# Performance work log

Hardware: AMD Instinct MI355X
Metric: run time of the kernel (lower is better)

Reference implementation:

```python
import jax, jax.numpy as jnp
import numpy as np

LN_EPS = 1e-5


def _pos_embed_2d(w, h, c, dtype=jnp.float32):
    # matches build_2d_sincos_position_embedding: meshgrid indexing='xy' -> (h, w) grids
    grid_w = jnp.arange(w, dtype=jnp.float32)
    grid_h = jnp.arange(h, dtype=jnp.float32)
    gw, gh = jnp.meshgrid(grid_w, grid_h, indexing='xy')  # each (h, w)
    pos_dim = c // 4
    omega = 1.0 / (10000.0 ** (jnp.arange(pos_dim, dtype=jnp.float32) / pos_dim))
    out_w = gw.reshape(-1, 1) * omega[None]  # (h*w, pos_dim)
    out_h = gh.reshape(-1, 1) * omega[None]
    pe = jnp.concatenate([jnp.sin(out_w), jnp.cos(out_w), jnp.sin(out_h), jnp.cos(out_h)], axis=1)
    return pe.astype(dtype)  # (h*w, c)


def setup_inputs() -> dict:
    key = jax.random.key(0)
    k1, k2 = jax.random.split(key)
    N, C, H, W = 16, 256, 40, 40
    x = jax.random.normal(k1, (N, C, H, W), dtype=jnp.float32)
    ln_w = jnp.ones((C,), dtype=jnp.float32)
    ln_b = jnp.zeros((C,), dtype=jnp.float32)
    qkv_w = jax.random.normal(k2, (3 * C, C), dtype=jnp.float32) * 0.02  # 1x1 conv weight
    qkv_b = jnp.zeros((3 * C,), dtype=jnp.float32)
    gamma = jnp.ones((1,), dtype=jnp.float32)
    return {"x": x, "ln_w": ln_w, "ln_b": ln_b, "qkv_w": qkv_w, "qkv_b": qkv_b, "gamma": gamma}


def reference(x, ln_w, ln_b, qkv_w, qkv_b, gamma):
    N, C, H, W = x.shape
    scale = C ** (-0.5)
    identity = x

    # LayerNorm over channels (computed in NHWC like the torch permute dance)
    xh = jnp.transpose(x, (0, 2, 3, 1))  # (N, H, W, C)
    mu = jnp.mean(xh, axis=-1, keepdims=True)
    var = jnp.mean(jnp.square(xh - mu), axis=-1, keepdims=True)
    xn = (xh - mu) * jax.lax.rsqrt(var + LN_EPS) * ln_w + ln_b

    # 1x1 conv == per-pixel linear
    qkv = jnp.einsum('nhwc,oc->nhwo', xn, qkv_w) + qkv_b  # (N, H, W, 3C)
    qkv = qkv.reshape(N, H * W, 3 * C)
    q, k, v = jnp.split(qkv, 3, axis=-1)  # each (N, HW, C)

    pe = _pos_embed_2d(W, H, C, x.dtype)  # (HW, C)
    q = q + pe
    k = k + pe

    attn = jax.nn.softmax(jnp.einsum('nqc,nkc->nqk', q, k) * scale, axis=-1)
    out = jnp.einsum('nqk,nkc->nqc', attn, v)  # (N, HW, C)
    out = jnp.transpose(out, (0, 2, 1)).reshape(N, C, H, W)
    return identity + gamma[0] * out
```

## Files before the change

kernel.cpp:

```cpp
#include <hip/hip_runtime.h>
#include <hip/hip_bf16.h>

typedef float f32x4 __attribute__((ext_vector_type(4)));
typedef float f32x16 __attribute__((ext_vector_type(16)));
typedef __bf16 v8bf __attribute__((ext_vector_type(8)));
typedef unsigned short ushortx4 __attribute__((ext_vector_type(4)));
typedef unsigned short ushortx8 __attribute__((ext_vector_type(8)));
typedef unsigned int uint4v __attribute__((ext_vector_type(4)));

#define NIMG 16
#define CCH  256
#define HWP  1600

#define QSCALE 0.09016844f
#define DEFER_THR 2.885390f

__device__ __forceinline__ unsigned short f2bf(float f) {
  unsigned int u = __builtin_bit_cast(unsigned int, f);
  u = (u + 0x7FFFu + ((u >> 16) & 1u)) >> 16;
  return (unsigned short)u;
}

__device__ __forceinline__ f32x4 mfma16(v8bf a, v8bf b, f32x4 c) {
  return __builtin_amdgcn_mfma_f32_16x16x32_bf16(a, b, c, 0, 0, 0);
}

__device__ __forceinline__ unsigned cvtpk(float a, float b) {
  unsigned r;
  asm("v_cvt_pk_bf16_f32 %0, %1, %2" : "=v"(r) : "v"(a), "v"(b));
  return r;
}
__device__ __forceinline__ float exp2v(float x) {
  float r;
  asm("v_exp_f32 %0, %1" : "=v"(r) : "v"(x));
  return r;
}
__device__ __forceinline__ float sin2pi(float rev) {
  float r;
  asm("v_fract_f32 %0, %1\n\tv_sin_f32 %0, %0" : "=v"(r) : "v"(rev));
  return r;
}
#define PSWAP(a, b) asm("v_permlane32_swap_b32 %0, %1" : "+v"(a), "+v"(b))

__global__ void prep_kernel(const float* __restrict__ qkv_w,
                            float* __restrict__ pe,
                            unsigned short* __restrict__ w_frag) {
  int tid = blockIdx.x * blockDim.x + threadIdx.x;
  int nthr = gridDim.x * blockDim.x;
  for (int i = tid; i < 768 * 256; i += nthr) {
    int o = i >> 8, c = i & 255;
    int tile = o >> 4, lr = o & 15;
    int ks = c >> 5, lg = (c >> 3) & 3, e = c & 7;
    w_frag[(((size_t)tile * 8 + ks) * 64 + lg * 16 + lr) * 8 + e] = f2bf(qkv_w[i]);
  }
  const float oc = 0.20762051f;
  const float inv2pi = 0.15915494f;
  for (int i = tid; i < HWP * 256; i += nthr) {
    int p = i >> 8, c = i & 255;
    int j = p % 40, ii = p / 40;
    int tt = c & 63;
    float omega = exp2v(-(float)tt * oc) * inv2pi;
    float coord = (c < 128) ? (float)j : (float)ii;
    float rev = coord * omega;
    if (c & 64) rev += 0.25f;
    pe[i] = sin2pi(rev);
  }
}

__global__ __launch_bounds__(512, 4) void ln_qkv_kernel(
    const float* __restrict__ x, const float* __restrict__ ln_w, const float* __restrict__ ln_b,
    const unsigned short* __restrict__ w_frag, const float* __restrict__ qkv_b,
    const float* __restrict__ pe,
    unsigned short* __restrict__ q_arr, unsigned short* __restrict__ k_arr,
    unsigned short* __restrict__ v_arr) {
  __shared__ unsigned short buf[64][256];
  __shared__ float red_s[8][64], red_q[8][64];
  __shared__ float mu_s[64], rs_s[64];

  int t = threadIdx.x;
  int n = blockIdx.x / 25, pt = blockIdx.x % 25;
  int pix0 = pt * 64;
  int p = t & 63, g = t >> 6;
  const float* xb = x + (size_t)n * CCH * HWP + pix0;

  {
    float sum = 0.f, sq = 0.f;
#pragma unroll
    for (int i = 0; i < 32; ++i) {
      float v = xb[(size_t)(g * 32 + i) * HWP + p];
      sum += v; sq += v * v;
    }
    red_s[g][p] = sum; red_q[g][p] = sq;
  }
  __syncthreads();
  if (t < 64) {
    float s = 0.f, q2 = 0.f;
#pragma unroll
    for (int gg = 0; gg < 8; ++gg) { s += red_s[gg][t]; q2 += red_q[gg][t]; }
    float mu = s * (1.f / 256.f);
    float var = q2 * (1.f / 256.f) - mu * mu;
    mu_s[t] = mu;
    rs_s[t] = rsqrtf(var + 1e-5f);
  }
  __syncthreads();
  {
    float mu = mu_s[p], rs = rs_s[p];
    int p7 = p & 7;
#pragma unroll
    for (int i4 = 0; i4 < 8; ++i4) {
      int c0 = g * 32 + i4 * 4;
      f32x4 lw = *(const f32x4*)&ln_w[c0];
      f32x4 lb = *(const f32x4*)&ln_b[c0];
      ushortx4 pk;
#pragma unroll
      for (int r = 0; r < 4; ++r) {
        float v = xb[(size_t)(c0 + r) * HWP + p];
        pk[r] = f2bf((v - mu) * rs * lw[r] + lb[r]);
      }
      int unit = (c0 >> 3) ^ p7;
      *(ushortx4*)&buf[p][unit * 8 + (i4 & 1) * 4] = pk;
    }
  }
  __syncthreads();

  int w = t >> 6, l = t & 63, lr = l & 15, lg = l >> 4;
  int lr7 = lr & 7;
  f32x4 acc[6][4];
#pragma unroll
  for (int nf = 0; nf < 6; ++nf)
#pragma unroll
    for (int mi = 0; mi < 4; ++mi) acc[nf][mi] = (f32x4){0.f, 0.f, 0.f, 0.f};

#pragma unroll
  for (int ks = 0; ks < 8; ++ks) {
    v8bf bF[4];
#pragma unroll
    for (int mi = 0; mi < 4; ++mi)
      bF[mi] = *(const v8bf*)&buf[mi * 16 + lr][((ks * 4 + lg) ^ lr7) * 8];
#pragma unroll
    for (int nf = 0; nf < 6; ++nf) {
      int tile = w + nf * 8;
      v8bf wf = *(const v8bf*)&w_frag[(((size_t)tile * 8 + ks) * 64 + l) * 8];
#pragma unroll
      for (int mi = 0; mi < 4; ++mi) acc[nf][mi] = mfma16(wf, bF[mi], acc[nf][mi]);
    }
  }

  int lgh = lg >> 1, lgl = lg & 1;
#pragma unroll
  for (int nf = 0; nf < 2; ++nf) {
    int tile = w + nf * 8;
    f32x4 bi = *(const f32x4*)&qkv_b[tile * 16 + lg * 4];
#pragma unroll
    for (int mi = 0; mi < 4; ++mi) {
      int pix = pix0 + mi * 16 + lr;
      f32x4 pev = *(const f32x4*)&pe[(size_t)pix * 256 + tile * 16 + lg * 4];
      f32x4 vv = (acc[nf][mi] + bi + pev) * QSCALE;
      ushortx4 pk = {f2bf(vv[0]), f2bf(vv[1]), f2bf(vv[2]), f2bf(vv[3])};
      int qt = pix >> 5, l31 = pix & 31;
      size_t ad = ((((size_t)n * 50 + qt) * 16 + tile) * 2 + lgh) * 256 + l31 * 8 + lgl * 4;
      *(ushortx4*)&q_arr[ad] = pk;
    }
  }
#pragma unroll
  for (int nf = 2; nf < 4; ++nf) {
    int tile = w + nf * 8;
    int dt = tile - 16;
    f32x4 bi = *(const f32x4*)&qkv_b[tile * 16 + lg * 4];
#pragma unroll
    for (int mi = 0; mi < 4; ++mi) {
      int pix = pix0 + mi * 16 + lr;
      f32x4 pev = *(const f32x4*)&pe[(size_t)pix * 256 + dt * 16 + lg * 4];
      f32x4 vv = acc[nf][mi] + bi + pev;
      ushortx4 pk = {f2bf(vv[0]), f2bf(vv[1]), f2bf(vv[2]), f2bf(vv[3])};
      size_t ad = (((size_t)n * 16 + dt) * 1600 + pix) * 16 + lgh * 8 + lgl * 4;
      *(ushortx4*)&k_arr[ad] = pk;
    }
  }
#pragma unroll
  for (int nf = 4; nf < 6; ++nf) {
    int tile = w + nf * 8;
    f32x4 bi = *(const f32x4*)&qkv_b[tile * 16 + lg * 4];
#pragma unroll
    for (int mi = 0; mi < 4; ++mi) {
      int pix = pix0 + mi * 16 + lr;
      int kvs = pix >> 4, hi = (pix >> 3) & 1, e = pix & 7;
      f32x4 vv = acc[nf][mi] + bi;
      size_t vb = (((size_t)n * 100 + kvs) * 2 + hi) * 2048 + e;
      int d0 = (tile - 32) * 16 + lg * 4;
#pragma unroll
      for (int r = 0; r < 4; ++r)
        v_arr[vb + (size_t)(d0 + r) * 8] = f2bf(vv[r]);
    }
  }
}

__global__ __launch_bounds__(128, 2) void attn_kernel(
    const unsigned short* __restrict__ q_arr, const unsigned short* __restrict__ k_arr,
    const unsigned short* __restrict__ v_arr, const float* __restrict__ x,
    const float* __restrict__ gamma, float* __restrict__ out) {
  __shared__ float sx[4][2][4][64][4];

  int t = threadIdx.x;
  int wv = t >> 6, l = t & 63;
  int l31 = l & 31, hi = l >> 5;
  int dto = wv * 8;
  int dto32 = wv * 4;
  int slot = blockIdx.x & 7, j = blockIdx.x >> 3;
  int n = slot + 8 * (j / 50);
  int qt = j % 50;
  int q0 = qt * 32;

  v8bf qf[8];
  {
    const unsigned short* qp = q_arr + (((size_t)n * 50 + qt) * 32 + hi) * 256 + l31 * 8;
#pragma unroll
    for (int i = 0; i < 8; ++i)
      qf[i] = *(const v8bf*)(qp + (dto + i) * 512);
  }

  f32x16 acc[4];
#pragma unroll
  for (int dd = 0; dd < 4; ++dd)
#pragma unroll
    for (int r = 0; r < 16; ++r) acc[dd][r] = 0.f;

  float m_run = -1e30f, l_run = 0.f;

  const unsigned short* kbase = k_arr + (size_t)n * (16 * 1600 * 16) +
                                (size_t)dto * 25600 + hi * 8;
  const unsigned short* vbase = v_arr + (size_t)n * (100 * 2 * 256 * 8) +
                                hi * 2048 + l31 * 8 + dto32 * 256;

  v8bf kc[8];
#pragma unroll
  for (int i = 0; i < 8; ++i)
    kc[i] = *(const v8bf*)(kbase + (size_t)i * 25600 + l31 * 16);

  f32x16 sA, sB;
#pragma unroll
  for (int r = 0; r < 16; ++r) sA[r] = 0.f;
#pragma unroll
  for (int i = 0; i < 8; ++i)
    sA = __builtin_amdgcn_mfma_f32_32x32x16_bf16(kc[i], qf[i], sA, 0, 0, 0);

#pragma unroll
  for (int r4 = 0; r4 < 4; ++r4) {
    f32x4 vv = {sA[r4 * 4 + 0], sA[r4 * 4 + 1], sA[r4 * 4 + 2], sA[r4 * 4 + 3]};
    *(f32x4*)&sx[0][wv][r4][l][0] = vv;
  }
#pragma unroll
  for (int i = 0; i < 8; ++i)
    kc[i] = *(const v8bf*)(kbase + (size_t)i * 25600 + (32 + l31) * 16);

  v8bf vf0[4], vf1[4];
#pragma unroll
  for (int i = 0; i < 4; ++i) vf0[i] = *(const v8bf*)(vbase + i * 256);
#pragma unroll
  for (int i = 0; i < 4; ++i) vf1[i] = *(const v8bf*)(vbase + 4096 + i * 256);

  auto body = [&](int kt, f32x16& scur, f32x16& snxt, bool nexttile) {
    __syncthreads();
    int br = kt & 3;
    float p[16];
#pragma unroll
    for (int r4 = 0; r4 < 4; ++r4) {
      f32x4 oth = *(const f32x4*)&sx[br][wv ^ 1][r4][l][0];
#pragma unroll
      for (int rr = 0; rr < 4; ++rr)
        p[r4 * 4 + rr] = scur[r4 * 4 + rr] + oth[rr];
    }
    if (nexttile) {
#pragma unroll
      for (int r = 0; r < 16; ++r) snxt[r] = 0.f;
#pragma unroll
      for (int i = 0; i < 4; ++i)
        snxt = __builtin_amdgcn_mfma_f32_32x32x16_bf16(kc[i], qf[i], snxt, 0, 0, 0);
    }
    float t0 = fmaxf(p[0], p[1]), t1 = fmaxf(p[2], p[3]);
    float t2 = fmaxf(p[4], p[5]), t3 = fmaxf(p[6], p[7]);
    float t4 = fmaxf(p[8], p[9]), t5 = fmaxf(p[10], p[11]);
    float t6 = fmaxf(p[12], p[13]), t7 = fmaxf(p[14], p[15]);
    float mx = fmaxf(fmaxf(fmaxf(t0, t1), fmaxf(t2, t3)),
                     fmaxf(fmaxf(t4, t5), fmaxf(t6, t7)));
    mx = fmaxf(mx, __shfl_xor(mx, 32));
    if (!__all(mx <= m_run + DEFER_THR)) {
      float mnew = fmaxf(m_run, mx);
      float alpha = exp2v(m_run - mnew);
      l_run *= alpha;
#pragma unroll
      for (int dd = 0; dd < 4; ++dd)
#pragma unroll
        for (int r = 0; r < 16; ++r) acc[dd][r] *= alpha;
      m_run = mnew;
    }
    if (nexttile) {
#pragma unroll
      for (int i = 4; i < 8; ++i)
        snxt = __builtin_amdgcn_mfma_f32_32x32x16_bf16(kc[i], qf[i], snxt, 0, 0, 0);
    }
#pragma unroll
    for (int r = 0; r < 16; ++r) p[r] = exp2v(p[r] - m_run);
    float sSum = ((p[0] + p[1]) + (p[2] + p[3])) + ((p[4] + p[5]) + (p[6] + p[7])) +
                 (((p[8] + p[9]) + (p[10] + p[11])) + ((p[12] + p[13]) + (p[14] + p[15])));
    sSum += __shfl_xor(sSum, 32);
    l_run += sSum;

    unsigned x0 = cvtpk(p[0], p[1]), x1 = cvtpk(p[2], p[3]);
    unsigned y0 = cvtpk(p[4], p[5]), y1 = cvtpk(p[6], p[7]);
    PSWAP(x0, y0); PSWAP(x1, y1);
    uint4v u0 = {x0, x1, y0, y1};
    v8bf pf0 = __builtin_bit_cast(v8bf, u0);
    unsigned z0 = cvtpk(p[8], p[9]), z1 = cvtpk(p[10], p[11]);
    unsigned w0 = cvtpk(p[12], p[13]), w1 = cvtpk(p[14], p[15]);
    PSWAP(z0, w0); PSWAP(z1, w1);
    uint4v u1 = {z0, z1, w0, w1};
    v8bf pf1 = __builtin_bit_cast(v8bf, u1);

#pragma unroll
    for (int dd = 0; dd < 4; ++dd) {
      acc[dd] = __builtin_amdgcn_mfma_f32_32x32x16_bf16(vf0[dd], pf0, acc[dd], 0, 0, 0);
      acc[dd] = __builtin_amdgcn_mfma_f32_32x32x16_bf16(vf1[dd], pf1, acc[dd], 0, 0, 0);
    }

    if (nexttile) {
      int bw = (kt + 1) & 3;
#pragma unroll
      for (int r4 = 0; r4 < 4; ++r4) {
        f32x4 vv = {snxt[r4 * 4 + 0], snxt[r4 * 4 + 1], snxt[r4 * 4 + 2], snxt[r4 * 4 + 3]};
        *(f32x4*)&sx[bw][wv][r4][l][0] = vv;
      }
      int kt2 = (kt + 2 < 50) ? kt + 2 : 0;
#pragma unroll
      for (int i = 0; i < 8; ++i)
        kc[i] = *(const v8bf*)(kbase + (size_t)i * 25600 + (kt2 * 32 + l31) * 16);
      const unsigned short* vp = vbase + (size_t)(kt + 1) * 8192;
#pragma unroll
      for (int i = 0; i < 4; ++i) vf0[i] = *(const v8bf*)(vp + i * 256);
#pragma unroll
      for (int i = 0; i < 4; ++i) vf1[i] = *(const v8bf*)(vp + 4096 + i * 256);
    }
  };

  for (int kt = 0; kt < 48; kt += 2) {
    body(kt, sA, sB, true);
    body(kt + 1, sB, sA, true);
  }
  body(48, sA, sB, true);
  body(49, sB, sA, false);

  float inv = 1.f / l_run;
  float gm = gamma[0];
#pragma unroll
  for (int dd = 0; dd < 4; ++dd) {
#pragma unroll
    for (int r = 0; r < 16; ++r) {
      int d = (dto32 + dd) * 32 + (r & 3) + 8 * (r >> 2) + 4 * hi;
      size_t base = ((size_t)n * 256 + d) * HWP + q0 + l31;
      out[base] = x[base] + gm * acc[dd][r] * inv;
    }
  }
}

extern "C" void kernel_launch(void* const* d_in, const int* in_sizes, int n_in,
                              void* d_out, int out_size, void* d_ws, size_t ws_size,
                              hipStream_t stream) {
  const float* x     = (const float*)d_in[0];
  const float* ln_w  = (const float*)d_in[1];
  const float* ln_b  = (const float*)d_in[2];
  const float* qkv_w = (const float*)d_in[3];
  const float* qkv_b = (const float*)d_in[4];
  const float* gamma = (const float*)d_in[5];
  float* out = (float*)d_out;

  char* ws = (char*)d_ws;
  unsigned short* w_frag = (unsigned short*)ws;
  float*          pe     = (float*)(ws + 393216);
  unsigned short* q_arr  = (unsigned short*)(ws + 2031616);
  unsigned short* k_arr  = (unsigned short*)(ws + 15138816);
  unsigned short* v_arr  = (unsigned short*)(ws + 28246016);

  hipLaunchKernelGGL(prep_kernel, dim3(1024), dim3(256), 0, stream, qkv_w, pe, w_frag);
  hipLaunchKernelGGL(ln_qkv_kernel, dim3(400), dim3(512), 0, stream,
                     x, ln_w, ln_b, w_frag, qkv_b, pe, q_arr, k_arr, v_arr);
  hipLaunchKernelGGL(attn_kernel, dim3(800), dim3(128), 0, stream,
                     q_arr, k_arr, v_arr, x, gamma, out);
}
```

Before: 125.8 us.

## Split attention head dimension across four waves instead of two

```diff
diff --git a/kernel.cpp b/kernel.cpp
--- a/kernel.cpp
+++ b/kernel.cpp
@@ -195,88 +195,91 @@
   }
 }
 
-__global__ __launch_bounds__(128, 2) void attn_kernel(
+__global__ __launch_bounds__(256, 2) void attn_kernel(
     const unsigned short* __restrict__ q_arr, const unsigned short* __restrict__ k_arr,
     const unsigned short* __restrict__ v_arr, const float* __restrict__ x,
     const float* __restrict__ gamma, float* __restrict__ out) {
-  __shared__ float sx[4][2][4][64][4];
+  __shared__ float sx[2][4][4][64][4];
 
   int t = threadIdx.x;
-  int wv = t >> 6, l = t & 63;
+  int dh = t >> 6, l = t & 63;
   int l31 = l & 31, hi = l >> 5;
-  int dto = wv * 8;
-  int dto32 = wv * 4;
   int slot = blockIdx.x & 7, j = blockIdx.x >> 3;
   int n = slot + 8 * (j / 50);
   int qt = j % 50;
   int q0 = qt * 32;
 
-  v8bf qf[8];
+  v8bf qf[4];
   {
     const unsigned short* qp = q_arr + (((size_t)n * 50 + qt) * 32 + hi) * 256 + l31 * 8;
 #pragma unroll
-    for (int i = 0; i < 8; ++i)
-      qf[i] = *(const v8bf*)(qp + (dto + i) * 512);
-  }
-
-  f32x16 acc[4];
-#pragma unroll
-  for (int dd = 0; dd < 4; ++dd)
-#pragma unroll
-    for (int r = 0; r < 16; ++r) acc[dd][r] = 0.f;
+    for (int i = 0; i < 4; ++i)
+      qf[i] = *(const v8bf*)(qp + (dh * 4 + i) * 512);
+  }
+
+  f32x16 acc0, acc1;
+#pragma unroll
+  for (int r = 0; r < 16; ++r) { acc0[r] = 0.f; acc1[r] = 0.f; }
 
   float m_run = -1e30f, l_run = 0.f;
 
   const unsigned short* kbase = k_arr + (size_t)n * (16 * 1600 * 16) +
-                                (size_t)dto * 25600 + hi * 8;
+                                (size_t)(dh * 4) * 25600 + hi * 8;
   const unsigned short* vbase = v_arr + (size_t)n * (100 * 2 * 256 * 8) +
-                                hi * 2048 + l31 * 8 + dto32 * 256;
-
-  v8bf kc[8];
-#pragma unroll
-  for (int i = 0; i < 8; ++i)
+                                hi * 2048 + l31 * 8 + (dh * 2) * 256;
+
+  v8bf kc[4];
+#pragma unroll
+  for (int i = 0; i < 4; ++i)
     kc[i] = *(const v8bf*)(kbase + (size_t)i * 25600 + l31 * 16);
 
-  f32x16 sA, sB;
-#pragma unroll
-  for (int r = 0; r < 16; ++r) sA[r] = 0.f;
-#pragma unroll
-  for (int i = 0; i < 8; ++i)
-    sA = __builtin_amdgcn_mfma_f32_32x32x16_bf16(kc[i], qf[i], sA, 0, 0, 0);
-
+  f32x16 s0, s1;
+#pragma unroll
+  for (int r = 0; r < 16; ++r) { s0[r] = 0.f; s1[r] = 0.f; }
+  s0 = __builtin_amdgcn_mfma_f32_32x32x16_bf16(kc[0], qf[0], s0, 0, 0, 0);
+  s1 = __builtin_amdgcn_mfma_f32_32x32x16_bf16(kc[1], qf[1], s1, 0, 0, 0);
+  s0 = __builtin_amdgcn_mfma_f32_32x32x16_bf16(kc[2], qf[2], s0, 0, 0, 0);
+  s1 = __builtin_amdgcn_mfma_f32_32x32x16_bf16(kc[3], qf[3], s1, 0, 0, 0);
 #pragma unroll
   for (int r4 = 0; r4 < 4; ++r4) {
-    f32x4 vv = {sA[r4 * 4 + 0], sA[r4 * 4 + 1], sA[r4 * 4 + 2], sA[r4 * 4 + 3]};
-    *(f32x4*)&sx[0][wv][r4][l][0] = vv;
-  }
-#pragma unroll
-  for (int i = 0; i < 8; ++i)
+    f32x4 vv = {s0[r4 * 4 + 0] + s1[r4 * 4 + 0], s0[r4 * 4 + 1] + s1[r4 * 4 + 1],
+                s0[r4 * 4 + 2] + s1[r4 * 4 + 2], s0[r4 * 4 + 3] + s1[r4 * 4 + 3]};
+    *(f32x4*)&sx[0][dh][r4][l][0] = vv;
+  }
+#pragma unroll
+  for (int i = 0; i < 4; ++i)
     kc[i] = *(const v8bf*)(kbase + (size_t)i * 25600 + (32 + l31) * 16);
 
-  v8bf vf0[4], vf1[4];
-#pragma unroll
-  for (int i = 0; i < 4; ++i) vf0[i] = *(const v8bf*)(vbase + i * 256);
-#pragma unroll
-  for (int i = 0; i < 4; ++i) vf1[i] = *(const v8bf*)(vbase + 4096 + i * 256);
-
-  auto body = [&](int kt, f32x16& scur, f32x16& snxt, bool nexttile) {
+  v8bf vf0[2], vf1[2];
+#pragma unroll
+  for (int i = 0; i < 2; ++i) vf0[i] = *(const v8bf*)(vbase + i * 256);
+#pragma unroll
+  for (int i = 0; i < 2; ++i) vf1[i] = *(const v8bf*)(vbase + 4096 + i * 256);
+
+  for (int kt = 0; kt < 50; ++kt) {
+    bool nexttile = (kt < 49);
     __syncthreads();
-    int br = kt & 3;
+    int br = kt & 1;
+
+    if (nexttile) {
+#pragma unroll
+      for (int r = 0; r < 16; ++r) { s0[r] = 0.f; s1[r] = 0.f; }
+      s0 = __builtin_amdgcn_mfma_f32_32x32x16_bf16(kc[0], qf[0], s0, 0, 0, 0);
+      s1 = __builtin_amdgcn_mfma_f32_32x32x16_bf16(kc[1], qf[1], s1, 0, 0, 0);
+    }
+
     float p[16];
 #pragma unroll
     for (int r4 = 0; r4 < 4; ++r4) {
-      f32x4 oth = *(const f32x4*)&sx[br][wv ^ 1][r4][l][0];
+      f32x4 a = *(const f32x4*)&sx[br][0][r4][l][0];
+      f32x4 b = *(const f32x4*)&sx[br][1][r4][l][0];
+      f32x4 c = *(const f32x4*)&sx[br][2][r4][l][0];
+      f32x4 d = *(const f32x4*)&sx[br][3][r4][l][0];
 #pragma unroll
       for (int rr = 0; rr < 4; ++rr)
-        p[r4 * 4 + rr] = scur[r4 * 4 + rr] + oth[rr];
-    }
-    if (nexttile) {
-#pragma unroll
-      for (int r = 0; r < 16; ++r) snxt[r] = 0.f;
-#pragma unroll
-      for (int i = 0; i < 4; ++i)
-        snxt = __builtin_amdgcn_mfma_f32_32x32x16_bf16(kc[i], qf[i], snxt, 0, 0, 0);
-    }
+        p[r4 * 4 + rr] = (a[rr] + b[rr]) + (c[rr] + d[rr]);
+    }
+
     float t0 = fmaxf(p[0], p[1]), t1 = fmaxf(p[2], p[3]);
     float t2 = fmaxf(p[4], p[5]), t3 = fmaxf(p[6], p[7]);
     float t4 = fmaxf(p[8], p[9]), t5 = fmaxf(p[10], p[11]);
@@ -289,16 +292,19 @@
       float alpha = exp2v(m_run - mnew);
       l_run *= alpha;
 #pragma unroll
-      for (int dd = 0; dd < 4; ++dd)
-#pragma unroll
-        for (int r = 0; r < 16; ++r) acc[dd][r] *= alpha;
+      for (int r = 0; r < 16; ++r) { acc0[r] *= alpha; acc1[r] *= alpha; }
       m_run = mnew;
     }
+
     if (nexttile) {
-#pragma unroll
-      for (int i = 4; i < 8; ++i)
-        snxt = __builtin_amdgcn_mfma_f32_32x32x16_bf16(kc[i], qf[i], snxt, 0, 0, 0);
-    }
+      s0 = __builtin_amdgcn_mfma_f32_32x32x16_bf16(kc[2], qf[2], s0, 0, 0, 0);
+      s1 = __builtin_amdgcn_mfma_f32_32x32x16_bf16(kc[3], qf[3], s1, 0, 0, 0);
+      int kt2 = (kt + 2 < 50) ? kt + 2 : 0;
+#pragma unroll
+      for (int i = 0; i < 4; ++i)
+        kc[i] = *(const v8bf*)(kbase + (size_t)i * 25600 + (kt2 * 32 + l31) * 16);
+    }
+
 #pragma unroll
     for (int r = 0; r < 16; ++r) p[r] = exp2v(p[r] - m_run);
     float sSum = ((p[0] + p[1]) + (p[2] + p[3])) + ((p[4] + p[5]) + (p[6] + p[7])) +
@@ -317,48 +323,39 @@
     uint4v u1 = {z0, z1, w0, w1};
     v8bf pf1 = __builtin_bit_cast(v8bf, u1);
 
-#pragma unroll
-    for (int dd = 0; dd < 4; ++dd) {
-      acc[dd] = __builtin_amdgcn_mfma_f32_32x32x16_bf16(vf0[dd], pf0, acc[dd], 0, 0, 0);
-      acc[dd] = __builtin_amdgcn_mfma_f32_32x32x16_bf16(vf1[dd], pf1, acc[dd], 0, 0, 0);
-    }
+    acc0 = __builtin_amdgcn_mfma_f32_32x32x16_bf16(vf0[0], pf0, acc0, 0, 0, 0);
+    acc1 = __builtin_amdgcn_mfma_f32_32x32x16_bf16(vf0[1], pf0, acc1, 0, 0, 0);
+    acc0 = __builtin_amdgcn_mfma_f32_32x32x16_bf16(vf1[0], pf1, acc0, 0, 0, 0);
+    acc1 = __builtin_amdgcn_mfma_f32_32x32x16_bf16(vf1[1], pf1, acc1, 0, 0, 0);
 
     if (nexttile) {
-      int bw = (kt + 1) & 3;
 #pragma unroll
       for (int r4 = 0; r4 < 4; ++r4) {
-        f32x4 vv = {snxt[r4 * 4 + 0], snxt[r4 * 4 + 1], snxt[r4 * 4 + 2], snxt[r4 * 4 + 3]};
-        *(f32x4*)&sx[bw][wv][r4][l][0] = vv;
+        f32x4 vv = {s0[r4 * 4 + 0] + s1[r4 * 4 + 0], s0[r4 * 4 + 1] + s1[r4 * 4 + 1],
+                    s0[r4 * 4 + 2] + s1[r4 * 4 + 2], s0[r4 * 4 + 3] + s1[r4 * 4 + 3]};
+        *(f32x4*)&sx[br ^ 1][dh][r4][l][0] = vv;
       }
-      int kt2 = (kt + 2 < 50) ? kt + 2 : 0;
-#pragma unroll
-      for (int i = 0; i < 8; ++i)
-        kc[i] = *(const v8bf*)(kbase + (size_t)i * 25600 + (kt2 * 32 + l31) * 16);
       const unsigned short* vp = vbase + (size_t)(kt + 1) * 8192;
 #pragma unroll
-      for (int i = 0; i < 4; ++i) vf0[i] = *(const v8bf*)(vp + i * 256);
-#pragma unroll
-      for (int i = 0; i < 4; ++i) vf1[i] = *(const v8bf*)(vp + 4096 + i * 256);
-    }
-  };
-
-  for (int kt = 0; kt < 48; kt += 2) {
-    body(kt, sA, sB, true);
-    body(kt + 1, sB, sA, true);
-  }
-  body(48, sA, sB, true);
-  body(49, sB, sA, false);
+      for (int i = 0; i < 2; ++i) vf0[i] = *(const v8bf*)(vp + i * 256);
+#pragma unroll
+      for (int i = 0; i < 2; ++i) vf1[i] = *(const v8bf*)(vp + 4096 + i * 256);
+    }
+  }
 
   float inv = 1.f / l_run;
   float gm = gamma[0];
 #pragma unroll
-  for (int dd = 0; dd < 4; ++dd) {
-#pragma unroll
-    for (int r = 0; r < 16; ++r) {
-      int d = (dto32 + dd) * 32 + (r & 3) + 8 * (r >> 2) + 4 * hi;
-      size_t base = ((size_t)n * 256 + d) * HWP + q0 + l31;
-      out[base] = x[base] + gm * acc[dd][r] * inv;
-    }
+  for (int r = 0; r < 16; ++r) {
+    int d = (dh * 2 + 0) * 32 + (r & 3) + 8 * (r >> 2) + 4 * hi;
+    size_t base = ((size_t)n * 256 + d) * HWP + q0 + l31;
+    out[base] = x[base] + gm * acc0[r] * inv;
+  }
+#pragma unroll
+  for (int r = 0; r < 16; ++r) {
+    int d = (dh * 2 + 1) * 32 + (r & 3) + 8 * (r >> 2) + 4 * hi;
+    size_t base = ((size_t)n * 256 + d) * HWP + q0 + l31;
+    out[base] = x[base] + gm * acc1[r] * inv;
   }
 }
 
@@ -383,6 +380,6 @@
   hipLaunchKernelGGL(prep_kernel, dim3(1024), dim3(256), 0, stream, qkv_w, pe, w_frag);
   hipLaunchKernelGGL(ln_qkv_kernel, dim3(400), dim3(512), 0, stream,
                      x, ln_w, ln_b, w_frag, qkv_b, pe, q_arr, k_arr, v_arr);
-  hipLaunchKernelGGL(attn_kernel, dim3(800), dim3(128), 0, stream,
+  hipLaunchKernelGGL(attn_kernel, dim3(800), dim3(256), 0, stream,
                      q_arr, k_arr, v_arr, x, gamma, out);
 }
```

New measurement: 173.0 us. +37.6%, slower.
